# Performance work log

Hardware: AMD Instinct MI355X
Metric: run time of the kernel (lower is better)

## Reference

```python
import jax, jax.numpy as jnp
import numpy as np

BATCH = 32768
INPUT_DIM = 256
N_NEURONS = 128
MAX_DEGREE = 7  # D; features per input dim = D+1 = 8


def _cheb_features(x, degree):
    """Chebyshev T_0..T_degree of x [B, In] -> [B, In, degree+1] via recurrence.

    Matches torch.special.chebyshev_polynomial_t(x, n=d) for d = 0..degree.
    """
    T = [jnp.ones_like(x), x]
    for _ in range(2, degree + 1):
        T.append(2.0 * x * T[-1] - T[-2])
    return jnp.stack(T[: degree + 1], axis=-1)


def setup_inputs() -> dict:
    key = jax.random.key(0)
    k1, k2 = jax.random.split(key)
    # inputs in [0,1) keep Chebyshev values bounded, as in a normalized pipeline
    x = jax.random.uniform(k1, (BATCH, INPUT_DIM), dtype=jnp.float32)
    # per-neuron coefficient vectors over the dim-major [In*(D+1)] feature layout
    coeffs = jax.random.normal(k2, (N_NEURONS, INPUT_DIM * (MAX_DEGREE + 1)), dtype=jnp.float32) * 0.02
    return {"x": x, "coeffs": coeffs}


def reference(x, coeffs):
    B, In = x.shape
    D = coeffs.shape[1] // In - 1
    # [B, In, D+1] -> dim-major flatten matches torch.cat over per-dim stacks
    X = _cheb_features(x, D).reshape(B, In * (D + 1))
    # per-neuron dot products, then sum over neurons (KANLayer stack().sum(0))
    per_neuron = jnp.einsum("bf,nf->bn", X, coeffs)  # [B, n_neurons]
    return per_neuron.sum(axis=1, keepdims=True)  # [B, 1]
```

## Files before the change

### kernel.cpp

```cpp
#include <hip/hip_runtime.h>

#define BATCH     32768
#define IN_DIM    256
#define N_NEURONS 128
#define DEG1      8
#define FEAT      (IN_DIM * DEG1)
#define F4        (FEAT / 4)
#define XR4       (IN_DIM / 4)
#define RPW       16

__global__ __launch_bounds__(256) void reduce_coeffs(const float* __restrict__ coeffs,
                                                     float* __restrict__ csum) {
    __shared__ float4 part[256];
    const int t = threadIdx.x;
    const int c = t & 7;
    const int g = t >> 3;
    const int col4 = blockIdx.x * 8 + c;

    const float4* p = (const float4*)coeffs + (size_t)(g * 4) * F4 + col4;
    float4 s = make_float4(0.f, 0.f, 0.f, 0.f);
#pragma unroll
    for (int n = 0; n < 4; ++n) {
        float4 v = p[(size_t)n * F4];
        s.x += v.x; s.y += v.y; s.z += v.z; s.w += v.w;
    }
    part[t] = s;
    __syncthreads();

#pragma unroll
    for (int stride = 128; stride >= 8; stride >>= 1) {
        if (t < stride) {
            float4 o = part[t + stride];
            float4 m = part[t];
            m.x += o.x; m.y += o.y; m.z += o.z; m.w += o.w;
            part[t] = m;
        }
        __syncthreads();
    }
    if (t < 8) ((float4*)csum)[blockIdx.x * 8 + t] = part[t];
}

__global__ __launch_bounds__(256) void kan_fwd(const float* __restrict__ x,
                                               const float* __restrict__ csum,
                                               float* __restrict__ out) {
    const int lane = threadIdx.x & 63;
    const int wave = threadIdx.x >> 6;
    const int row0 = (blockIdx.x * 4 + wave) * RPW;

    float c[4][8];
    const float4* c4 = (const float4*)csum + (size_t)lane * 8;
#pragma unroll
    for (int j = 0; j < 4; ++j) {
        float4 a = c4[j * 2];
        float4 b = c4[j * 2 + 1];
        c[j][0] = a.x; c[j][1] = a.y; c[j][2] = a.z; c[j][3] = a.w;
        c[j][4] = b.x; c[j][5] = b.y; c[j][6] = b.z; c[j][7] = b.w;
    }

    float acc[RPW];
    const float4* xr = (const float4*)x + (size_t)row0 * XR4 + lane;

#pragma unroll
    for (int r = 0; r < RPW; ++r) {
        float4 xv = xr[(size_t)r * XR4];
        float xs[4] = {xv.x, xv.y, xv.z, xv.w};
        float a = 0.f;
#pragma unroll
        for (int j = 0; j < 4; ++j) {
            const float xx = xs[j];
            const float two_x = xx + xx;
            a = fmaf(c[j][1], xx, a + c[j][0]);
            float tp = 1.f, tc = xx;
#pragma unroll
            for (int d = 2; d < 8; ++d) {
                float tn = fmaf(two_x, tc, -tp);
                a = fmaf(c[j][d], tn, a);
                tp = tc; tc = tn;
            }
        }
        acc[r] = a;
    }

#pragma unroll
    for (int rq = 0; rq < RPW / 4; ++rq) {
        float s[4];
#pragma unroll
        for (int k = 0; k < 4; ++k) {
            float a = acc[rq * 4 + k];
#pragma unroll
            for (int off = 32; off > 0; off >>= 1) a += __shfl_down(a, off, 64);
            s[k] = a;
        }
        if (lane == 0) {
            ((float4*)out)[row0 / 4 + rq] = make_float4(s[0], s[1], s[2], s[3]);
        }
    }
}

extern "C" void kernel_launch(void* const* d_in, const int* in_sizes, int n_in,
                              void* d_out, int out_size, void* d_ws, size_t ws_size,
                              hipStream_t stream) {
    const float* x      = (const float*)d_in[0];
    const float* coeffs = (const float*)d_in[1];
    float* out  = (float*)d_out;
    float* csum = (float*)d_ws;

    reduce_coeffs<<<64, 256, 0, stream>>>(coeffs, csum);
    kan_fwd<<<BATCH / (4 * RPW), 256, 0, stream>>>(x, csum, out);
}
```

Baseline: 77.69 us.

## Fuse coefficient reduction and forward pass into one cooperative kernel

Replaces the two launches (coefficient column reduction, then the per-row Chebyshev evaluation) with a single cooperative kernel. The first 64 blocks do the reduction, every block prefetches its x rows into registers, and a grid-wide sync then publishes the reduced coefficients. The aim is to remove the second launch and overlap x loads with the reduction. The cost is a grid barrier, fewer rows per wave (8 instead of 16) across 1024 blocks, and a fallback to the old path if the cooperative launch fails.

```diff
diff --git a/kernel.cpp b/kernel.cpp
--- a/kernel.cpp
+++ b/kernel.cpp
@@ -1,4 +1,7 @@
 #include <hip/hip_runtime.h>
+#include <hip/hip_cooperative_groups.h>
+
+namespace cg = cooperative_groups;
 
 #define BATCH     32768
 #define IN_DIM    256
@@ -8,6 +11,8 @@
 #define F4        (FEAT / 4)
 #define XR4       (IN_DIM / 4)
 #define RPW       16
+#define RPW_F     8
+#define NBLK_F    1024
 
 __global__ __launch_bounds__(256) void reduce_coeffs(const float* __restrict__ coeffs,
                                                      float* __restrict__ csum) {
@@ -26,7 +31,6 @@
     }
     part[t] = s;
     __syncthreads();
-
 #pragma unroll
     for (int stride = 128; stride >= 8; stride >>= 1) {
         if (t < stride) {
@@ -59,7 +63,6 @@
 
     float acc[RPW];
     const float4* xr = (const float4*)x + (size_t)row0 * XR4 + lane;
-
 #pragma unroll
     for (int r = 0; r < RPW; ++r) {
         float4 xv = xr[(size_t)r * XR4];
@@ -91,9 +94,101 @@
             for (int off = 32; off > 0; off >>= 1) a += __shfl_down(a, off, 64);
             s[k] = a;
         }
-        if (lane == 0) {
+        if (lane == 0)
             ((float4*)out)[row0 / 4 + rq] = make_float4(s[0], s[1], s[2], s[3]);
-        }
+    }
+}
+
+__global__ __launch_bounds__(256) void kan_fused(const float* __restrict__ x,
+                                                 const float* __restrict__ coeffs,
+                                                 float* __restrict__ out,
+                                                 float* __restrict__ csum) {
+    cg::grid_group grid = cg::this_grid();
+
+    const int lane = threadIdx.x & 63;
+    const int wave = threadIdx.x >> 6;
+    const int row0 = (blockIdx.x * 4 + wave) * RPW_F;
+
+    __shared__ float4 part[256];
+
+    if (blockIdx.x < 64) {
+        const int t = threadIdx.x;
+        const int c = t & 7;
+        const int g = t >> 3;
+        const int col4 = blockIdx.x * 8 + c;
+        const float4* p = (const float4*)coeffs + (size_t)(g * 4) * F4 + col4;
+        float4 s = make_float4(0.f, 0.f, 0.f, 0.f);
+#pragma unroll
+        for (int n = 0; n < 4; ++n) {
+            float4 v = p[(size_t)n * F4];
+            s.x += v.x; s.y += v.y; s.z += v.z; s.w += v.w;
+        }
+        part[t] = s;
+        __syncthreads();
+#pragma unroll
+        for (int stride = 128; stride >= 8; stride >>= 1) {
+            if (t < stride) {
+                float4 o = part[t + stride];
+                float4 m = part[t];
+                m.x += o.x; m.y += o.y; m.z += o.z; m.w += o.w;
+                part[t] = m;
+            }
+            __syncthreads();
+        }
+        if (t < 8) ((float4*)csum)[blockIdx.x * 8 + t] = part[t];
+        __threadfence();
+    }
+
+    float4 xv[RPW_F];
+    const float4* xr = (const float4*)x + (size_t)row0 * XR4 + lane;
+#pragma unroll
+    for (int r = 0; r < RPW_F; ++r) xv[r] = xr[(size_t)r * XR4];
+
+    grid.sync();
+
+    float c[4][8];
+    const float4* c4 = (const float4*)csum + (size_t)lane * 8;
+#pragma unroll
+    for (int j = 0; j < 4; ++j) {
+        float4 a = c4[j * 2];
+        float4 b = c4[j * 2 + 1];
+        c[j][0] = a.x; c[j][1] = a.y; c[j][2] = a.z; c[j][3] = a.w;
+        c[j][4] = b.x; c[j][5] = b.y; c[j][6] = b.z; c[j][7] = b.w;
+    }
+
+    float acc[RPW_F];
+#pragma unroll
+    for (int r = 0; r < RPW_F; ++r) {
+        float xs[4] = {xv[r].x, xv[r].y, xv[r].z, xv[r].w};
+        float a = 0.f;
+#pragma unroll
+        for (int j = 0; j < 4; ++j) {
+            const float xx = xs[j];
+            const float two_x = xx + xx;
+            a = fmaf(c[j][1], xx, a + c[j][0]);
+            float tp = 1.f, tc = xx;
+#pragma unroll
+            for (int d = 2; d < 8; ++d) {
+                float tn = fmaf(two_x, tc, -tp);
+                a = fmaf(c[j][d], tn, a);
+                tp = tc; tc = tn;
+            }
+        }
+        acc[r] = a;
+    }
+
+#pragma unroll
+    for (int rq = 0; rq < RPW_F / 4; ++rq) {
+        float s[4];
+#pragma unroll
+        for (int k = 0; k < 4; ++k) {
+            float a = acc[rq * 4 + k];
+#pragma unroll
+            for (int off = 32; off > 0; off >>= 1) a += __shfl_down(a, off, 64);
+            s[k] = a;
+        }
+        if (lane == 0)
+            ((float4*)out)[row0 / 4 + rq] = make_float4(s[0], s[1], s[2], s[3]);
     }
 }
 
@@ -105,6 +200,12 @@
     float* out  = (float*)d_out;
     float* csum = (float*)d_ws;
 
-    reduce_coeffs<<<64, 256, 0, stream>>>(coeffs, csum);
-    kan_fwd<<<BATCH / (4 * RPW), 256, 0, stream>>>(x, csum, out);
-}
+    void* args[] = {(void*)&x, (void*)&coeffs, (void*)&out, (void*)&csum};
+    hipError_t err = hipLaunchCooperativeKernel((const void*)kan_fused,
+                                                dim3(NBLK_F), dim3(256),
+                                                args, 0, stream);
+    if (err != hipSuccess) {
+        reduce_coeffs<<<64, 256, 0, stream>>>(coeffs, csum);
+        kan_fwd<<<BATCH / (4 * RPW), 256, 0, stream>>>(x, csum, out);
+    }
+}
```

Measured after the change: 181.8 us. +134.1%, slower.
